# Kernel tuning notes

Measured on AMD Instinct MI355X. Metric: run time of the kernel, lower is better.

## Reference

```python
import jax, jax.numpy as jnp
import numpy as np
import math

B, T, D = 4, 8192, 1024
EPS = 1e-5

def setup_inputs() -> dict:
    key = jax.random.key(0)
    ks = jax.random.split(key, 8)
    xavier = lambda k, shape: jax.random.uniform(k, shape, jnp.float32,
                                                 -math.sqrt(6.0 / (shape[0] + shape[1])),
                                                 math.sqrt(6.0 / (shape[0] + shape[1])))
    x = jax.random.normal(ks[0], (B, T, D), jnp.float32)
    ln_gamma = jnp.ones((D,), jnp.float32)
    ln_beta = jnp.zeros((D,), jnp.float32)
    Wg = xavier(ks[1], (D, D))            # torch Linear weight: (out, in)
    bg = jnp.zeros((D,), jnp.float32)
    Wv = 0.01 * xavier(ks[2], (D, D))     # gain=0.01
    bv = jnp.zeros((D,), jnp.float32)
    Wo = 0.01 * xavier(ks[3], (D, D))     # gain=0.01
    bo = jnp.zeros((D,), jnp.float32)
    log_decay = jnp.asarray(math.log(math.exp(0.01) - 1.0), jnp.float32)
    return {"x": x, "ln_gamma": ln_gamma, "ln_beta": ln_beta,
            "Wg": Wg, "bg": bg, "Wv": Wv, "bv": bv, "Wo": Wo, "bo": bo,
            "log_decay": log_decay}

def reference(x, ln_gamma, ln_beta, Wg, bg, Wv, bv, Wo, bo, log_decay):
    # LayerNorm
    mu = jnp.mean(x, axis=-1, keepdims=True)
    var = jnp.mean(jnp.square(x - mu), axis=-1, keepdims=True)
    normed = (x - mu) * jax.lax.rsqrt(var + EPS) * ln_gamma + ln_beta
    # gate / value projections (torch Linear: y = x @ W.T + b)
    g = jax.nn.sigmoid(jnp.einsum('btd,ed->bte', normed, Wg) + bg)
    v = jnp.einsum('btd,ed->bte', normed, Wv) + bv
    # push-pull cumulative sums over time
    cumsum = jnp.cumsum(g * v, axis=1) - jnp.cumsum((1.0 - g) * v, axis=1)
    # positional exponential decay
    alpha = jax.nn.softplus(log_decay)
    positions = jnp.arange(x.shape[1], dtype=jnp.float32)
    decay = jnp.exp(-alpha * positions)[None, :, None]  # (1,T,1)
    out = jnp.einsum('btd,ed->bte', cumsum * decay, Wo) + bo
    return x + out  # dropout is identity at eval
```

## Files before the change

### kernel.cpp

```cpp
#include <hip/hip_runtime.h>
#include <cstdint>
#include <cstddef>

#define DD 1024
#define TT 8192
#define BB 4
#define MM (BB*TT)
#define NCHUNK 64
#define CLEN 128
#define EPS 1e-5f
#define NKT 32

typedef __attribute__((ext_vector_type(8))) short bf16x8;
typedef __attribute__((ext_vector_type(4))) float f32x4;

__device__ __forceinline__ float bf2f(unsigned short b) {
  union { unsigned int u; float f; } c; c.u = ((unsigned int)b) << 16; return c.f;
}
__device__ __forceinline__ unsigned short f2bf(float f) {
  union { float f; unsigned int u; } c; c.f = f;
  unsigned int lsb = (c.u >> 16) & 1u;
  c.u += 0x7fffu + lsb;
  return (unsigned short)(c.u >> 16);
}

__device__ __forceinline__ void gload16(const void* gsrc, void* ldst) {
  __builtin_amdgcn_global_load_lds(
      (const __attribute__((address_space(1))) unsigned int*)gsrc,
      (__attribute__((address_space(3))) unsigned int*)ldst, 16, 0, 0);
}

#define SWZ(row) (((row) >> 1) & 3)

template<int R>
__device__ __forceinline__ void stageT(const unsigned short* __restrict__ g,
                                       size_t row0, int k0,
                                       unsigned short* lds, int tid) {
#pragma unroll
  for (int l = 0; l < R / 128; ++l) {
    int u16 = l * 512 + tid;
    int row = u16 >> 2;
    int sp  = u16 & 3;
    int sl  = sp ^ SWZ(row);
    const unsigned short* src = g + (row0 + (size_t)row) * DD + k0 + sl * 8;
    gload16(src, (char*)lds + (size_t)u16 * 16);
  }
}

__device__ __forceinline__ bf16x8 ldsfrag(const unsigned short* lds, int row, int sl) {
  int sp = sl ^ SWZ(row);
  return *(const bf16x8*)&lds[row * 32 + sp * 8];
}

__device__ __forceinline__ void phase_barrier() {
  __builtin_amdgcn_sched_barrier(0);
  __builtin_amdgcn_s_barrier();
  __builtin_amdgcn_sched_barrier(0);
}
template<int N>
__device__ __forceinline__ void tile_barrier_vm() {
  __builtin_amdgcn_sched_barrier(0);
  if constexpr (N == 4) asm volatile("s_waitcnt vmcnt(4)" ::: "memory");
  else                  asm volatile("s_waitcnt vmcnt(0)" ::: "memory");
  __builtin_amdgcn_s_barrier();
  __builtin_amdgcn_sched_barrier(0);
}

__global__ __launch_bounds__(256) void cast_weights(
    const float* __restrict__ wg, const float* __restrict__ wv,
    const float* __restrict__ wo,
    unsigned short* __restrict__ owg, unsigned short* __restrict__ owv,
    unsigned short* __restrict__ owo) {
  int i = blockIdx.x * 256 + threadIdx.x;
  const float* src; unsigned short* dst; int off;
  if (i < 262144)       { src = wg; dst = owg; off = i; }
  else if (i < 524288)  { src = wv; dst = owv; off = i - 262144; }
  else                  { src = wo; dst = owo; off = i - 524288; }
  float4 v = ((const float4*)src)[off];
  ushort4 o;
  o.x = f2bf(v.x); o.y = f2bf(v.y); o.z = f2bf(v.z); o.w = f2bf(v.w);
  ((ushort4*)dst)[off] = o;
}

__global__ __launch_bounds__(256) void ln_kernel(
    const float* __restrict__ x, const float* __restrict__ gamma,
    const float* __restrict__ beta, unsigned short* __restrict__ normed) {
  size_t row = blockIdx.x;
  int tid = threadIdx.x, lane = tid & 63, wid = tid >> 6;
  float4 v = ((const float4*)(x + row * DD))[tid];
  float s = v.x + v.y + v.z + v.w;
  float q = v.x * v.x + v.y * v.y + v.z * v.z + v.w * v.w;
#pragma unroll
  for (int off = 32; off; off >>= 1) {
    s += __shfl_down(s, off);
    q += __shfl_down(q, off);
  }
  __shared__ float rs[4], rq[4];
  if (lane == 0) { rs[wid] = s; rq[wid] = q; }
  __syncthreads();
  float ts = rs[0] + rs[1] + rs[2] + rs[3];
  float tq = rq[0] + rq[1] + rq[2] + rq[3];
  float mu  = ts * (1.0f / DD);
  float var = tq * (1.0f / DD) - mu * mu;
  float rstd = rsqrtf(var + EPS);
  float4 gm = ((const float4*)gamma)[tid];
  float4 bt = ((const float4*)beta)[tid];
  ushort4 o;
  o.x = f2bf((v.x - mu) * rstd * gm.x + bt.x);
  o.y = f2bf((v.y - mu) * rstd * gm.y + bt.y);
  o.z = f2bf((v.z - mu) * rstd * gm.z + bt.z);
  o.w = f2bf((v.w - mu) * rstd * gm.w + bt.w);
  ((ushort4*)normed)[row * (DD / 4) + tid] = o;
}

__global__ __launch_bounds__(512, 2) void gemm_gv(
    const unsigned short* __restrict__ normed,
    const unsigned short* __restrict__ wg, const unsigned short* __restrict__ wv,
    const float* __restrict__ bg, const float* __restrict__ bv,
    unsigned short* __restrict__ u) {
  __shared__ unsigned short As[4][256 * 32];
  __shared__ unsigned short Bgs[4][128 * 32];
  __shared__ unsigned short Bvs[4][128 * 32];
  int tid = threadIdx.x, lane = tid & 63, wid = tid >> 6;
  int wm = wid & 3, wn = wid >> 2;
  int nwg = gridDim.x;
  int swz = (blockIdx.x & 7) * (nwg >> 3) + (blockIdx.x >> 3);
  int bx = swz & 127;
  int by = swz >> 7;
  size_t m0 = (size_t)bx * 256;
  int n0 = by * 128;

  f32x4 accg[4][4], accv[4][4];
#pragma unroll
  for (int a = 0; a < 4; ++a)
#pragma unroll
    for (int b = 0; b < 4; ++b) {
      accg[a][b] = (f32x4){0.f, 0.f, 0.f, 0.f};
      accv[a][b] = (f32x4){0.f, 0.f, 0.f, 0.f};
    }

  stageT<256>(normed, m0, 0, As[0], tid);
  stageT<128>(wg, (size_t)n0, 0, Bgs[0], tid);
  stageT<128>(wv, (size_t)n0, 0, Bvs[0], tid);
  stageT<256>(normed, m0, 32, As[1], tid);
  stageT<128>(wg, (size_t)n0, 32, Bgs[1], tid);
  stageT<128>(wv, (size_t)n0, 32, Bvs[1], tid);
  tile_barrier_vm<4>();

  int r = lane & 15, sl = lane >> 4;
  for (int kt = 0; kt < NKT; ++kt) {
    int buf = kt & 3;
    bf16x8 af[4];
#pragma unroll
    for (int mi = 0; mi < 4; ++mi)
      af[mi] = ldsfrag(As[buf], wm * 64 + mi * 16 + r, sl);
    bf16x8 bgf[4];
#pragma unroll
    for (int ni = 0; ni < 4; ++ni)
      bgf[ni] = ldsfrag(Bgs[buf], wn * 64 + ni * 16 + r, sl);
    if (kt < NKT - 2)
      stageT<256>(normed, m0, (kt + 2) * 32, As[(kt + 2) & 3], tid);
    phase_barrier();
    __builtin_amdgcn_s_setprio(1);
#pragma unroll
    for (int ni = 0; ni < 4; ++ni)
#pragma unroll
      for (int mi = 0; mi < 4; ++mi)
        accg[mi][ni] = __builtin_amdgcn_mfma_f32_16x16x32_bf16(af[mi], bgf[ni], accg[mi][ni], 0, 0, 0);
    __builtin_amdgcn_s_setprio(0);
    phase_barrier();
    bf16x8 bvf[4];
#pragma unroll
    for (int ni = 0; ni < 4; ++ni)
      bvf[ni] = ldsfrag(Bvs[buf], wn * 64 + ni * 16 + r, sl);
    if (kt < NKT - 2) {
      stageT<128>(wg, (size_t)n0, (kt + 2) * 32, Bgs[(kt + 2) & 3], tid);
      stageT<128>(wv, (size_t)n0, (kt + 2) * 32, Bvs[(kt + 2) & 3], tid);
    }
    phase_barrier();
    __builtin_amdgcn_s_setprio(1);
#pragma unroll
    for (int ni = 0; ni < 4; ++ni)
#pragma unroll
      for (int mi = 0; mi < 4; ++mi)
        accv[mi][ni] = __builtin_amdgcn_mfma_f32_16x16x32_bf16(af[mi], bvf[ni], accv[mi][ni], 0, 0, 0);
    __builtin_amdgcn_s_setprio(0);
    if (kt < NKT - 2) tile_barrier_vm<4>();
    else              tile_barrier_vm<0>();
  }

#pragma unroll
  for (int mi = 0; mi < 4; ++mi)
#pragma unroll
    for (int ni = 0; ni < 4; ++ni) {
      int e = n0 + wn * 64 + ni * 16 + (lane & 15);
      size_t rbase = m0 + wm * 64 + mi * 16 + (lane >> 4) * 4;
      float bgv = bg[e], bvv = bv[e];
#pragma unroll
      for (int j = 0; j < 4; ++j) {
        float gp = accg[mi][ni][j] + bgv;
        float vp = accv[mi][ni][j] + bvv;
        float sg = 1.0f / (1.0f + __expf(-gp));
        float uu = (2.0f * sg - 1.0f) * vp;
        u[(rbase + j) * DD + e] = f2bf(uu);
      }
    }
}

__global__ __launch_bounds__(128) void scan_partial(
    const unsigned short* __restrict__ u, float* __restrict__ sums) {
  int bid = blockIdx.x;
  int half = bid & 1, chunk = (bid >> 1) & 63, b = bid >> 7;
  int e0 = half * 512 + threadIdx.x * 4;
  float a0 = 0.f, a1 = 0.f, a2 = 0.f, a3 = 0.f;
  size_t base = ((size_t)b * TT + (size_t)chunk * CLEN) * DD + e0;
#pragma unroll 4
  for (int i = 0; i < CLEN; ++i) {
    ushort4 w = *(const ushort4*)(u + base + (size_t)i * DD);
    a0 += bf2f(w.x); a1 += bf2f(w.y); a2 += bf2f(w.z); a3 += bf2f(w.w);
  }
  float4 rr; rr.x = a0; rr.y = a1; rr.z = a2; rr.w = a3;
  *(float4*)(sums + ((size_t)(b * NCHUNK + chunk)) * DD + e0) = rr;
}

__global__ __launch_bounds__(256) void scan_chunks(float* __restrict__ sums) {
  int b = blockIdx.x >> 2;
  int e = (blockIdx.x & 3) * 256 + threadIdx.x;
  float vals[NCHUNK];
#pragma unroll
  for (int c = 0; c < NCHUNK; ++c)
    vals[c] = sums[((size_t)(b * NCHUNK + c)) * DD + e];
  float carry = 0.f;
#pragma unroll
  for (int c = 0; c < NCHUNK; ++c) {
    float t = vals[c]; vals[c] = carry; carry += t;
  }
#pragma unroll
  for (int c = 0; c < NCHUNK; ++c)
    sums[((size_t)(b * NCHUNK + c)) * DD + e] = vals[c];
}

__global__ __launch_bounds__(128) void scan_final(
    unsigned short* __restrict__ u, const float* __restrict__ sums,
    const float* __restrict__ log_decay) {
  int bid = blockIdx.x;
  int half = bid & 1, chunk = (bid >> 1) & 63, b = bid >> 7;
  int e0 = half * 512 + threadIdx.x * 4;
  float alpha = log1pf(__expf(log_decay[0]));
  float4 c = *(const float4*)(sums + ((size_t)(b * NCHUNK + chunk)) * DD + e0);
  size_t base = ((size_t)b * TT + (size_t)chunk * CLEN) * DD + e0;
#pragma unroll 4
  for (int i = 0; i < CLEN; ++i) {
    int t = chunk * CLEN + i;
    float dec = __expf(-alpha * (float)t);
    ushort4 w = *(const ushort4*)(u + base + (size_t)i * DD);
    c.x += bf2f(w.x); c.y += bf2f(w.y); c.z += bf2f(w.z); c.w += bf2f(w.w);
    ushort4 o;
    o.x = f2bf(c.x * dec); o.y = f2bf(c.y * dec);
    o.z = f2bf(c.z * dec); o.w = f2bf(c.w * dec);
    *(ushort4*)(u + base + (size_t)i * DD) = o;
  }
}

__global__ __launch_bounds__(512, 2) void gemm_out(
    const unsigned short* __restrict__ cmat, const unsigned short* __restrict__ wo,
    const float* __restrict__ bo, const float* __restrict__ x,
    float* __restrict__ out) {
  __shared__ unsigned short As[4][256 * 32];
  __shared__ unsigned short Bs[4][256 * 32];
  int tid = threadIdx.x, lane = tid & 63, wid = tid >> 6;
  int wm = wid & 1, wn = wid >> 1;
  int nwg = gridDim.x;
  int swz = (blockIdx.x & 7) * (nwg >> 3) + (blockIdx.x >> 3);
  int bx = swz & 127;
  int by = swz >> 7;
  size_t m0 = (size_t)bx * 256;
  int n0 = by * 256;

  f32x4 acc[8][4];
#pragma unroll
  for (int a = 0; a < 8; ++a)
#pragma unroll
    for (int b = 0; b < 4; ++b) acc[a][b] = (f32x4){0.f, 0.f, 0.f, 0.f};

  stageT<256>(cmat, m0, 0, As[0], tid);
  stageT<256>(wo, (size_t)n0, 0, Bs[0], tid);
  stageT<256>(cmat, m0, 32, As[1], tid);
  stageT<256>(wo, (size_t)n0, 32, Bs[1], tid);
  tile_barrier_vm<4>();

  int r = lane & 15, sl = lane >> 4;
  for (int kt = 0; kt < NKT; ++kt) {
    int buf = kt & 3;
    bf16x8 af[8];
#pragma unroll
    for (int mi = 0; mi < 8; ++mi)
      af[mi] = ldsfrag(As[buf], wm * 128 + mi * 16 + r, sl);
    bf16x8 b0 = ldsfrag(Bs[buf], wn * 64 + 0 * 16 + r, sl);
    bf16x8 b1 = ldsfrag(Bs[buf], wn * 64 + 1 * 16 + r, sl);
    if (kt < NKT - 2)
      stageT<256>(cmat, m0, (kt + 2) * 32, As[(kt + 2) & 3], tid);
    phase_barrier();
    __builtin_amdgcn_s_setprio(1);
#pragma unroll
    for (int mi = 0; mi < 8; ++mi) {
      acc[mi][0] = __builtin_amdgcn_mfma_f32_16x16x32_bf16(af[mi], b0, acc[mi][0], 0, 0, 0);
      acc[mi][1] = __builtin_amdgcn_mfma_f32_16x16x32_bf16(af[mi], b1, acc[mi][1], 0, 0, 0);
    }
    __builtin_amdgcn_s_setprio(0);
    phase_barrier();
    bf16x8 b2 = ldsfrag(Bs[buf], wn * 64 + 2 * 16 + r, sl);
    bf16x8 b3 = ldsfrag(Bs[buf], wn * 64 + 3 * 16 + r, sl);
    if (kt < NKT - 2)
      stageT<256>(wo, (size_t)n0, (kt + 2) * 32, Bs[(kt + 2) & 3], tid);
    phase_barrier();
    __builtin_amdgcn_s_setprio(1);
#pragma unroll
    for (int mi = 0; mi < 8; ++mi) {
      acc[mi][2] = __builtin_amdgcn_mfma_f32_16x16x32_bf16(af[mi], b2, acc[mi][2], 0, 0, 0);
      acc[mi][3] = __builtin_amdgcn_mfma_f32_16x16x32_bf16(af[mi], b3, acc[mi][3], 0, 0, 0);
    }
    __builtin_amdgcn_s_setprio(0);
    if (kt < NKT - 2) tile_barrier_vm<4>();
    else              tile_barrier_vm<0>();
  }

#pragma unroll
  for (int mi = 0; mi < 8; ++mi)
#pragma unroll
    for (int ni = 0; ni < 4; ++ni) {
      int e = n0 + wn * 64 + ni * 16 + (lane & 15);
      size_t rbase = m0 + wm * 128 + mi * 16 + (lane >> 4) * 4;
      float bov = bo[e];
#pragma unroll
      for (int j = 0; j < 4; ++j) {
        size_t idx = (rbase + j) * DD + e;
        out[idx] = x[idx] + bov + acc[mi][ni][j];
      }
    }
}

extern "C" void kernel_launch(void* const* d_in, const int* in_sizes, int n_in,
                              void* d_out, int out_size, void* d_ws, size_t ws_size,
                              hipStream_t stream) {
  const float* x     = (const float*)d_in[0];
  const float* gamma = (const float*)d_in[1];
  const float* beta  = (const float*)d_in[2];
  const float* Wg    = (const float*)d_in[3];
  const float* bg    = (const float*)d_in[4];
  const float* Wv    = (const float*)d_in[5];
  const float* bv    = (const float*)d_in[6];
  const float* Wo    = (const float*)d_in[7];
  const float* bo    = (const float*)d_in[8];
  const float* ldcy  = (const float*)d_in[9];
  float* out = (float*)d_out;

  char* ws = (char*)d_ws;
  unsigned short* normed = (unsigned short*)ws;
  unsigned short* u      = (unsigned short*)(ws + (size_t)67108864);
  unsigned short* wgb    = (unsigned short*)(ws + (size_t)134217728);
  unsigned short* wvb    = wgb + 1048576;
  unsigned short* wob    = wvb + 1048576;
  float* sums            = (float*)(ws + (size_t)134217728 + (size_t)3 * 2097152);

  cast_weights<<<3072, 256, 0, stream>>>(Wg, Wv, Wo, wgb, wvb, wob);
  ln_kernel<<<MM, 256, 0, stream>>>(x, gamma, beta, normed);
  gemm_gv<<<dim3(MM / 256 * (DD / 128)), 512, 0, stream>>>(normed, wgb, wvb, bg, bv, u);
  scan_partial<<<BB * NCHUNK * 2, 128, 0, stream>>>(u, sums);
  scan_chunks<<<BB * (DD / 256), 256, 0, stream>>>(sums);
  scan_final<<<BB * NCHUNK * 2, 128, 0, stream>>>(u, sums, ldcy);
  gemm_out<<<dim3(MM / 256 * (DD / 256)), 512, 0, stream>>>(u, wob, bo, x, out);
}
```

Baseline: 387.1 us.

## Fuse chunk partial sums into gate/value GEMM and restructure K-loop pipelining

The scan_partial kernel is removed. Its per-chunk column sums are now computed in the gate/value GEMM epilogue through a wave-level shuffle reduction over the fp32 u values, which avoids re-reading u from global memory. Both GEMMs switch to a 64-wide K step with double buffering over two 32-wide sub-tiles, a new warp layout (8x2 fragments per wave), and reordered block swizzling that walks N fastest. The change adds explicit lgkmcnt waits. The chunk sums now come from unrounded fp32 values rather than the bf16-rounded u that scan_final reads, which adds a small numeric mismatch.

Result: faster. 328.3 us (-15.2%).

```diff
diff --git a/kernel.cpp b/kernel.cpp
--- a/kernel.cpp
+++ b/kernel.cpp
@@ -9,7 +9,7 @@
 #define NCHUNK 64
 #define CLEN 128
 #define EPS 1e-5f
-#define NKT 32
+#define NK2 16
 
 typedef __attribute__((ext_vector_type(8))) short bf16x8;
 typedef __attribute__((ext_vector_type(4))) float f32x4;
@@ -52,17 +52,10 @@
   return *(const bf16x8*)&lds[row * 32 + sp * 8];
 }
 
-__device__ __forceinline__ void phase_barrier() {
-  __builtin_amdgcn_sched_barrier(0);
-  __builtin_amdgcn_s_barrier();
-  __builtin_amdgcn_sched_barrier(0);
-}
-template<int N>
-__device__ __forceinline__ void tile_barrier_vm() {
-  __builtin_amdgcn_sched_barrier(0);
-  if constexpr (N == 4) asm volatile("s_waitcnt vmcnt(4)" ::: "memory");
-  else                  asm volatile("s_waitcnt vmcnt(0)" ::: "memory");
-  __builtin_amdgcn_s_barrier();
+#define MFMA16(a, b, c) __builtin_amdgcn_mfma_f32_16x16x32_bf16((a), (b), (c), 0, 0, 0)
+
+__device__ __forceinline__ void lgkm0_fence() {
+  asm volatile("s_waitcnt lgkmcnt(0)" ::: "memory");
   __builtin_amdgcn_sched_barrier(0);
 }
 
@@ -117,84 +110,119 @@
     const unsigned short* __restrict__ normed,
     const unsigned short* __restrict__ wg, const unsigned short* __restrict__ wv,
     const float* __restrict__ bg, const float* __restrict__ bv,
-    unsigned short* __restrict__ u) {
-  __shared__ unsigned short As[4][256 * 32];
-  __shared__ unsigned short Bgs[4][128 * 32];
-  __shared__ unsigned short Bvs[4][128 * 32];
+    unsigned short* __restrict__ u, float* __restrict__ sums) {
+  __shared__ unsigned short As[2][2][256 * 32];
+  __shared__ unsigned short Bgs[2][2][128 * 32];
+  __shared__ unsigned short Bvs[2][2][128 * 32];
   int tid = threadIdx.x, lane = tid & 63, wid = tid >> 6;
-  int wm = wid & 3, wn = wid >> 2;
+  int wm = wid >> 2, wn = wid & 3;
   int nwg = gridDim.x;
   int swz = (blockIdx.x & 7) * (nwg >> 3) + (blockIdx.x >> 3);
-  int bx = swz & 127;
-  int by = swz >> 7;
+  int bx = swz >> 3;
+  int by = swz & 7;
   size_t m0 = (size_t)bx * 256;
   int n0 = by * 128;
 
-  f32x4 accg[4][4], accv[4][4];
-#pragma unroll
-  for (int a = 0; a < 4; ++a)
-#pragma unroll
-    for (int b = 0; b < 4; ++b) {
+  f32x4 accg[8][2], accv[8][2];
+#pragma unroll
+  for (int a = 0; a < 8; ++a)
+#pragma unroll
+    for (int b = 0; b < 2; ++b) {
       accg[a][b] = (f32x4){0.f, 0.f, 0.f, 0.f};
       accv[a][b] = (f32x4){0.f, 0.f, 0.f, 0.f};
     }
 
-  stageT<256>(normed, m0, 0, As[0], tid);
-  stageT<128>(wg, (size_t)n0, 0, Bgs[0], tid);
-  stageT<128>(wv, (size_t)n0, 0, Bvs[0], tid);
-  stageT<256>(normed, m0, 32, As[1], tid);
-  stageT<128>(wg, (size_t)n0, 32, Bgs[1], tid);
-  stageT<128>(wv, (size_t)n0, 32, Bvs[1], tid);
-  tile_barrier_vm<4>();
-
-  int r = lane & 15, sl = lane >> 4;
-  for (int kt = 0; kt < NKT; ++kt) {
-    int buf = kt & 3;
-    bf16x8 af[4];
-#pragma unroll
-    for (int mi = 0; mi < 4; ++mi)
-      af[mi] = ldsfrag(As[buf], wm * 64 + mi * 16 + r, sl);
-    bf16x8 bgf[4];
-#pragma unroll
-    for (int ni = 0; ni < 4; ++ni)
-      bgf[ni] = ldsfrag(Bgs[buf], wn * 64 + ni * 16 + r, sl);
-    if (kt < NKT - 2)
-      stageT<256>(normed, m0, (kt + 2) * 32, As[(kt + 2) & 3], tid);
-    phase_barrier();
-    __builtin_amdgcn_s_setprio(1);
-#pragma unroll
-    for (int ni = 0; ni < 4; ++ni)
-#pragma unroll
-      for (int mi = 0; mi < 4; ++mi)
-        accg[mi][ni] = __builtin_amdgcn_mfma_f32_16x16x32_bf16(af[mi], bgf[ni], accg[mi][ni], 0, 0, 0);
-    __builtin_amdgcn_s_setprio(0);
-    phase_barrier();
-    bf16x8 bvf[4];
-#pragma unroll
-    for (int ni = 0; ni < 4; ++ni)
-      bvf[ni] = ldsfrag(Bvs[buf], wn * 64 + ni * 16 + r, sl);
-    if (kt < NKT - 2) {
-      stageT<128>(wg, (size_t)n0, (kt + 2) * 32, Bgs[(kt + 2) & 3], tid);
-      stageT<128>(wv, (size_t)n0, (kt + 2) * 32, Bvs[(kt + 2) & 3], tid);
-    }
-    phase_barrier();
-    __builtin_amdgcn_s_setprio(1);
-#pragma unroll
-    for (int ni = 0; ni < 4; ++ni)
-#pragma unroll
-      for (int mi = 0; mi < 4; ++mi)
-        accv[mi][ni] = __builtin_amdgcn_mfma_f32_16x16x32_bf16(af[mi], bvf[ni], accv[mi][ni], 0, 0, 0);
-    __builtin_amdgcn_s_setprio(0);
-    if (kt < NKT - 2) tile_barrier_vm<4>();
-    else              tile_barrier_vm<0>();
-  }
-
-#pragma unroll
-  for (int mi = 0; mi < 4; ++mi)
-#pragma unroll
-    for (int ni = 0; ni < 4; ++ni) {
-      int e = n0 + wn * 64 + ni * 16 + (lane & 15);
-      size_t rbase = m0 + wm * 64 + mi * 16 + (lane >> 4) * 4;
+  stageT<256>(normed, m0, 0,  As[0][0], tid);
+  stageT<128>(wg, (size_t)n0, 0,  Bgs[0][0], tid);
+  stageT<128>(wv, (size_t)n0, 0,  Bvs[0][0], tid);
+  stageT<256>(normed, m0, 32, As[0][1], tid);
+  stageT<128>(wg, (size_t)n0, 32, Bgs[0][1], tid);
+  stageT<128>(wv, (size_t)n0, 32, Bvs[0][1], tid);
+  asm volatile("s_waitcnt vmcnt(4)" ::: "memory");
+  __builtin_amdgcn_s_barrier();
+
+  int r = lane & 15, q = lane >> 4;
+  for (int t = 0; t < NK2; ++t) {
+    int buf = t & 1;
+    int k1 = (t + 1) * 64;
+    bool more = (t + 1 < NK2);
+    bf16x8 af[8], b0, b1;
+#pragma unroll
+    for (int mi = 0; mi < 8; ++mi)
+      af[mi] = ldsfrag(As[buf][0], wm * 128 + mi * 16 + r, q);
+    b0 = ldsfrag(Bgs[buf][0], wn * 32 + r, q);
+    b1 = ldsfrag(Bgs[buf][0], wn * 32 + 16 + r, q);
+    if (more) stageT<256>(normed, m0, k1, As[buf ^ 1][0], tid);
+    __builtin_amdgcn_s_barrier();
+    lgkm0_fence();
+    __builtin_amdgcn_s_setprio(1);
+#pragma unroll
+    for (int mi = 0; mi < 8; ++mi) {
+      accg[mi][0] = MFMA16(af[mi], b0, accg[mi][0]);
+      accg[mi][1] = MFMA16(af[mi], b1, accg[mi][1]);
+    }
+    __builtin_amdgcn_s_setprio(0);
+    __builtin_amdgcn_s_barrier();
+    b0 = ldsfrag(Bvs[buf][0], wn * 32 + r, q);
+    b1 = ldsfrag(Bvs[buf][0], wn * 32 + 16 + r, q);
+    if (more) {
+      stageT<128>(wg, (size_t)n0, k1, Bgs[buf ^ 1][0], tid);
+      stageT<128>(wv, (size_t)n0, k1, Bvs[buf ^ 1][0], tid);
+    }
+    __builtin_amdgcn_s_barrier();
+    lgkm0_fence();
+    __builtin_amdgcn_s_setprio(1);
+#pragma unroll
+    for (int mi = 0; mi < 8; ++mi) {
+      accv[mi][0] = MFMA16(af[mi], b0, accv[mi][0]);
+      accv[mi][1] = MFMA16(af[mi], b1, accv[mi][1]);
+    }
+    __builtin_amdgcn_s_setprio(0);
+    if (more) asm volatile("s_waitcnt vmcnt(4)" ::: "memory");
+    else      asm volatile("s_waitcnt vmcnt(0)" ::: "memory");
+    __builtin_amdgcn_s_barrier();
+#pragma unroll
+    for (int mi = 0; mi < 8; ++mi)
+      af[mi] = ldsfrag(As[buf][1], wm * 128 + mi * 16 + r, q);
+    b0 = ldsfrag(Bvs[buf][1], wn * 32 + r, q);
+    b1 = ldsfrag(Bvs[buf][1], wn * 32 + 16 + r, q);
+    if (more) stageT<256>(normed, m0, k1 + 32, As[buf ^ 1][1], tid);
+    __builtin_amdgcn_s_barrier();
+    lgkm0_fence();
+    __builtin_amdgcn_s_setprio(1);
+#pragma unroll
+    for (int mi = 0; mi < 8; ++mi) {
+      accv[mi][0] = MFMA16(af[mi], b0, accv[mi][0]);
+      accv[mi][1] = MFMA16(af[mi], b1, accv[mi][1]);
+    }
+    __builtin_amdgcn_s_setprio(0);
+    __builtin_amdgcn_s_barrier();
+    b0 = ldsfrag(Bgs[buf][1], wn * 32 + r, q);
+    b1 = ldsfrag(Bgs[buf][1], wn * 32 + 16 + r, q);
+    if (more) {
+      stageT<128>(wg, (size_t)n0, k1 + 32, Bgs[buf ^ 1][1], tid);
+      stageT<128>(wv, (size_t)n0, k1 + 32, Bvs[buf ^ 1][1], tid);
+    }
+    __builtin_amdgcn_s_barrier();
+    lgkm0_fence();
+    __builtin_amdgcn_s_setprio(1);
+#pragma unroll
+    for (int mi = 0; mi < 8; ++mi) {
+      accg[mi][0] = MFMA16(af[mi], b0, accg[mi][0]);
+      accg[mi][1] = MFMA16(af[mi], b1, accg[mi][1]);
+    }
+    __builtin_amdgcn_s_setprio(0);
+    if (more) asm volatile("s_waitcnt vmcnt(4)" ::: "memory");
+    __builtin_amdgcn_s_barrier();
+  }
+
+  float psum[2] = {0.f, 0.f};
+#pragma unroll
+  for (int mi = 0; mi < 8; ++mi)
+#pragma unroll
+    for (int ni = 0; ni < 2; ++ni) {
+      int e = n0 + wn * 32 + ni * 16 + r;
+      size_t rbase = m0 + wm * 128 + mi * 16 + q * 4;
       float bgv = bg[e], bvv = bv[e];
 #pragma unroll
       for (int j = 0; j < 4; ++j) {
@@ -202,25 +230,22 @@
         float vp = accv[mi][ni][j] + bvv;
         float sg = 1.0f / (1.0f + __expf(-gp));
         float uu = (2.0f * sg - 1.0f) * vp;
+        psum[ni] += uu;
         u[(rbase + j) * DD + e] = f2bf(uu);
       }
     }
-}
-
-__global__ __launch_bounds__(128) void scan_partial(
-    const unsigned short* __restrict__ u, float* __restrict__ sums) {
-  int bid = blockIdx.x;
-  int half = bid & 1, chunk = (bid >> 1) & 63, b = bid >> 7;
-  int e0 = half * 512 + threadIdx.x * 4;
-  float a0 = 0.f, a1 = 0.f, a2 = 0.f, a3 = 0.f;
-  size_t base = ((size_t)b * TT + (size_t)chunk * CLEN) * DD + e0;
-#pragma unroll 4
-  for (int i = 0; i < CLEN; ++i) {
-    ushort4 w = *(const ushort4*)(u + base + (size_t)i * DD);
-    a0 += bf2f(w.x); a1 += bf2f(w.y); a2 += bf2f(w.z); a3 += bf2f(w.w);
-  }
-  float4 rr; rr.x = a0; rr.y = a1; rr.z = a2; rr.w = a3;
-  *(float4*)(sums + ((size_t)(b * NCHUNK + chunk)) * DD + e0) = rr;
+#pragma unroll
+  for (int ni = 0; ni < 2; ++ni) {
+    psum[ni] += __shfl_xor(psum[ni], 16);
+    psum[ni] += __shfl_xor(psum[ni], 32);
+  }
+  if (lane < 16) {
+    int b = (int)(m0 >> 13);
+    int ch = (int)((m0 & 8191) >> 7) + wm;
+    size_t sidx = ((size_t)(b * NCHUNK + ch)) * DD + n0 + wn * 32 + lane;
+    sums[sidx]      = psum[0];
+    sums[sidx + 16] = psum[1];
+  }
 }
 
 __global__ __launch_bounds__(256) void scan_chunks(float* __restrict__ sums) {
@@ -266,14 +291,14 @@
     const unsigned short* __restrict__ cmat, const unsigned short* __restrict__ wo,
     const float* __restrict__ bo, const float* __restrict__ x,
     float* __restrict__ out) {
-  __shared__ unsigned short As[4][256 * 32];
-  __shared__ unsigned short Bs[4][256 * 32];
+  __shared__ unsigned short As[2][2][256 * 32];
+  __shared__ unsigned short Bs[2][2][256 * 32];
   int tid = threadIdx.x, lane = tid & 63, wid = tid >> 6;
-  int wm = wid & 1, wn = wid >> 1;
+  int wm = wid >> 2, wn = wid & 3;
   int nwg = gridDim.x;
   int swz = (blockIdx.x & 7) * (nwg >> 3) + (blockIdx.x >> 3);
-  int bx = swz & 127;
-  int by = swz >> 7;
+  int bx = swz >> 2;
+  int by = swz & 3;
   size_t m0 = (size_t)bx * 256;
   int n0 = by * 256;
 
@@ -283,59 +308,93 @@
 #pragma unroll
     for (int b = 0; b < 4; ++b) acc[a][b] = (f32x4){0.f, 0.f, 0.f, 0.f};
 
-  stageT<256>(cmat, m0, 0, As[0], tid);
-  stageT<256>(wo, (size_t)n0, 0, Bs[0], tid);
-  stageT<256>(cmat, m0, 32, As[1], tid);
-  stageT<256>(wo, (size_t)n0, 32, Bs[1], tid);
-  tile_barrier_vm<4>();
-
-  int r = lane & 15, sl = lane >> 4;
-  for (int kt = 0; kt < NKT; ++kt) {
-    int buf = kt & 3;
-    bf16x8 af[8];
+  stageT<256>(cmat, m0, 0,  As[0][0], tid);
+  stageT<256>(wo, (size_t)n0, 0,  Bs[0][0], tid);
+  stageT<256>(cmat, m0, 32, As[0][1], tid);
+  stageT<256>(wo, (size_t)n0, 32, Bs[0][1], tid);
+  asm volatile("s_waitcnt vmcnt(4)" ::: "memory");
+  __builtin_amdgcn_s_barrier();
+
+  int r = lane & 15, q = lane >> 4;
+  for (int t = 0; t < NK2; ++t) {
+    int buf = t & 1;
+    int k1 = (t + 1) * 64;
+    bool more = (t + 1 < NK2);
+    bf16x8 af[8], b0, b1;
 #pragma unroll
     for (int mi = 0; mi < 8; ++mi)
-      af[mi] = ldsfrag(As[buf], wm * 128 + mi * 16 + r, sl);
-    bf16x8 b0 = ldsfrag(Bs[buf], wn * 64 + 0 * 16 + r, sl);
-    bf16x8 b1 = ldsfrag(Bs[buf], wn * 64 + 1 * 16 + r, sl);
-    if (kt < NKT - 2)
-      stageT<256>(cmat, m0, (kt + 2) * 32, As[(kt + 2) & 3], tid);
-    phase_barrier();
-    __builtin_amdgcn_s_setprio(1);
-#pragma unroll
-    for (int mi = 0; mi < 8; ++mi) {
-      acc[mi][0] = __builtin_amdgcn_mfma_f32_16x16x32_bf16(af[mi], b0, acc[mi][0], 0, 0, 0);
-      acc[mi][1] = __builtin_amdgcn_mfma_f32_16x16x32_bf16(af[mi], b1, acc[mi][1], 0, 0, 0);
-    }
-    __builtin_amdgcn_s_setprio(0);
-    phase_barrier();
-    bf16x8 b2 = ldsfrag(Bs[buf], wn * 64 + 2 * 16 + r, sl);
-    bf16x8 b3 = ldsfrag(Bs[buf], wn * 64 + 3 * 16 + r, sl);
-    if (kt < NKT - 2)
-      stageT<256>(wo, (size_t)n0, (kt + 2) * 32, Bs[(kt + 2) & 3], tid);
-    phase_barrier();
-    __builtin_amdgcn_s_setprio(1);
-#pragma unroll
-    for (int mi = 0; mi < 8; ++mi) {
-      acc[mi][2] = __builtin_amdgcn_mfma_f32_16x16x32_bf16(af[mi], b2, acc[mi][2], 0, 0, 0);
-      acc[mi][3] = __builtin_amdgcn_mfma_f32_16x16x32_bf16(af[mi], b3, acc[mi][3], 0, 0, 0);
-    }
-    __builtin_amdgcn_s_setprio(0);
-    if (kt < NKT - 2) tile_barrier_vm<4>();
-    else              tile_barrier_vm<0>();
+      af[mi] = ldsfrag(As[buf][0], wm * 128 + mi * 16 + r, q);
+    b0 = ldsfrag(Bs[buf][0], wn * 64 + r, q);
+    b1 = ldsfrag(Bs[buf][0], wn * 64 + 16 + r, q);
+    if (more) stageT<256>(cmat, m0, k1, As[buf ^ 1][0], tid);
+    __builtin_amdgcn_s_barrier();
+    lgkm0_fence();
+    __builtin_amdgcn_s_setprio(1);
+#pragma unroll
+    for (int mi = 0; mi < 8; ++mi) {
+      acc[mi][0] = MFMA16(af[mi], b0, acc[mi][0]);
+      acc[mi][1] = MFMA16(af[mi], b1, acc[mi][1]);
+    }
+    __builtin_amdgcn_s_setprio(0);
+    __builtin_amdgcn_s_barrier();
+    b0 = ldsfrag(Bs[buf][0], wn * 64 + 32 + r, q);
+    b1 = ldsfrag(Bs[buf][0], wn * 64 + 48 + r, q);
+    if (more) stageT<256>(wo, (size_t)n0, k1, Bs[buf ^ 1][0], tid);
+    __builtin_amdgcn_s_barrier();
+    lgkm0_fence();
+    __builtin_amdgcn_s_setprio(1);
+#pragma unroll
+    for (int mi = 0; mi < 8; ++mi) {
+      acc[mi][2] = MFMA16(af[mi], b0, acc[mi][2]);
+      acc[mi][3] = MFMA16(af[mi], b1, acc[mi][3]);
+    }
+    __builtin_amdgcn_s_setprio(0);
+    if (more) asm volatile("s_waitcnt vmcnt(4)" ::: "memory");
+    else      asm volatile("s_waitcnt vmcnt(0)" ::: "memory");
+    __builtin_amdgcn_s_barrier();
+#pragma unroll
+    for (int mi = 0; mi < 8; ++mi)
+      af[mi] = ldsfrag(As[buf][1], wm * 128 + mi * 16 + r, q);
+    b0 = ldsfrag(Bs[buf][1], wn * 64 + 32 + r, q);
+    b1 = ldsfrag(Bs[buf][1], wn * 64 + 48 + r, q);
+    if (more) stageT<256>(cmat, m0, k1 + 32, As[buf ^ 1][1], tid);
+    __builtin_amdgcn_s_barrier();
+    lgkm0_fence();
+    __builtin_amdgcn_s_setprio(1);
+#pragma unroll
+    for (int mi = 0; mi < 8; ++mi) {
+      acc[mi][2] = MFMA16(af[mi], b0, acc[mi][2]);
+      acc[mi][3] = MFMA16(af[mi], b1, acc[mi][3]);
+    }
+    __builtin_amdgcn_s_setprio(0);
+    __builtin_amdgcn_s_barrier();
+    b0 = ldsfrag(Bs[buf][1], wn * 64 + r, q);
+    b1 = ldsfrag(Bs[buf][1], wn * 64 + 16 + r, q);
+    if (more) stageT<256>(wo, (size_t)n0, k1 + 32, Bs[buf ^ 1][1], tid);
+    __builtin_amdgcn_s_barrier();
+    lgkm0_fence();
+    __builtin_amdgcn_s_setprio(1);
+#pragma unroll
+    for (int mi = 0; mi < 8; ++mi) {
+      acc[mi][0] = MFMA16(af[mi], b0, acc[mi][0]);
+      acc[mi][1] = MFMA16(af[mi], b1, acc[mi][1]);
+    }
+    __builtin_amdgcn_s_setprio(0);
+    if (more) asm volatile("s_waitcnt vmcnt(4)" ::: "memory");
+    __builtin_amdgcn_s_barrier();
   }
 
 #pragma unroll
   for (int mi = 0; mi < 8; ++mi)
 #pragma unroll
-    for (int ni = 0; ni < 4; ++ni) {
-      int e = n0 + wn * 64 + ni * 16 + (lane & 15);
-      size_t rbase = m0 + wm * 128 + mi * 16 + (lane >> 4) * 4;
+    for (int nq = 0; nq < 4; ++nq) {
+      int e = n0 + wn * 64 + nq * 16 + r;
+      size_t rbase = m0 + wm * 128 + mi * 16 + q * 4;
       float bov = bo[e];
 #pragma unroll
       for (int j = 0; j < 4; ++j) {
         size_t idx = (rbase + j) * DD + e;
-        out[idx] = x[idx] + bov + acc[mi][ni][j];
+        out[idx] = x[idx] + bov + acc[mi][nq][j];
       }
     }
 }
@@ -365,8 +424,7 @@
 
   cast_weights<<<3072, 256, 0, stream>>>(Wg, Wv, Wo, wgb, wvb, wob);
   ln_kernel<<<MM, 256, 0, stream>>>(x, gamma, beta, normed);
-  gemm_gv<<<dim3(MM / 256 * (DD / 128)), 512, 0, stream>>>(normed, wgb, wvb, bg, bv, u);
-  scan_partial<<<BB * NCHUNK * 2, 128, 0, stream>>>(u, sums);
+  gemm_gv<<<dim3(MM / 256 * (DD / 128)), 512, 0, stream>>>(normed, wgb, wvb, bg, bv, u, sums);
   scan_chunks<<<BB * (DD / 256), 256, 0, stream>>>(sums);
   scan_final<<<BB * NCHUNK * 2, 128, 0, stream>>>(u, sums, ldcy);
   gemm_out<<<dim3(MM / 256 * (DD / 256)), 512, 0, stream>>>(u, wob, bo, x, out);
```
